# Optimization experiments

Measured on AMD Instinct MI355X. Metric: run time of the kernel, lower is better.

## Reference

```python
import jax, jax.numpy as jnp
import numpy as np
from jax import lax

EPS = 1e-5
HEADS = 4
NPOINT = 512


def _layernorm(x, g, b):
    mu = jnp.mean(x, axis=-1, keepdims=True)
    var = jnp.var(x, axis=-1, keepdims=True)
    return (x - mu) * lax.rsqrt(var + EPS) * g + b


def farthest_point_sample(xyz, npoint):
    # xyz: [B, N, 3] -> idx [B, npoint]  (canonical PointNet++ FPS, seeded at point 0)
    B, N, _ = xyz.shape

    def step(carry, _):
        dist, far = carry  # [B,N], [B]
        centroid = jnp.take_along_axis(xyz, far[:, None, None], axis=1)  # [B,1,3]
        d = jnp.sum((xyz - centroid) ** 2, axis=-1)  # [B,N]
        dist = jnp.minimum(dist, d)
        nxt = jnp.argmax(dist, axis=1).astype(jnp.int32)
        return (dist, nxt), far

    init = (jnp.full((B, N), 1e10, xyz.dtype), jnp.zeros((B,), jnp.int32))
    _, idx = lax.scan(step, init, None, length=npoint)  # [npoint, B]
    return idx.T  # [B, npoint]


def index_points(points, idx):
    # points: [B, N, D], idx: [B, S] -> [B, S, D]
    return jnp.take_along_axis(points, idx[..., None], axis=1)


def setup_inputs() -> dict:
    key = jax.random.key(0)
    ks = iter(jax.random.split(key, 16))
    B, N, Cin, D, Dff, Dout = 8, 2048, 64, 128, 512, 256
    w = lambda k, s: (jax.random.normal(k, s, jnp.float32) * 0.02)
    inp = {
        "xyz": jax.random.normal(next(ks), (B, 3, N), jnp.float32),
        "points": jax.random.normal(next(ks), (B, Cin, N), jnp.float32),
        "W_proj": w(next(ks), (D, Cin)), "b_proj": jnp.zeros((D,)),
        "bn1_g": jnp.ones((D,)), "bn1_b": jnp.zeros((D,)),
        "bn1_m": jnp.zeros((D,)), "bn1_v": jnp.ones((D,)),
        "W_pos": w(next(ks), (D, 3)), "b_pos": jnp.zeros((D,)),
        "Wq": w(next(ks), (D, D)), "bq": jnp.zeros((D,)),
        "Wk": w(next(ks), (D, D)), "bk": jnp.zeros((D,)),
        "Wv": w(next(ks), (D, D)), "bv": jnp.zeros((D,)),
        "Wo": w(next(ks), (D, D)), "bo": jnp.zeros((D,)),
        "ln1_g": jnp.ones((D,)), "ln1_b": jnp.zeros((D,)),
        "W1": w(next(ks), (Dff, D)), "b1": jnp.zeros((Dff,)),
        "W2": w(next(ks), (D, Dff)), "b2": jnp.zeros((D,)),
        "ln2_g": jnp.ones((D,)), "ln2_b": jnp.zeros((D,)),
        "W_fc": w(next(ks), (Dout, D + 3)), "b_fc": jnp.zeros((Dout,)),
        "bn2_g": jnp.ones((Dout,)), "bn2_b": jnp.zeros((Dout,)),
        "bn2_m": jnp.zeros((Dout,)), "bn2_v": jnp.ones((Dout,)),
    }
    return inp


def reference(xyz, points, W_proj, b_proj, bn1_g, bn1_b, bn1_m, bn1_v,
              W_pos, b_pos, Wq, bq, Wk, bk, Wv, bv, Wo, bo,
              ln1_g, ln1_b, W1, b1, W2, b2, ln2_g, ln2_b,
              W_fc, b_fc, bn2_g, bn2_b, bn2_m, bn2_v):
    B, _, N = xyz.shape
    D = W_proj.shape[0]
    hd = D // HEADS

    # project: pointwise conv + BN (inference), output [B, N, D]
    feat = jnp.einsum('dc,bcn->bnd', W_proj, points) + b_proj
    feat = (feat - bn1_m) * lax.rsqrt(bn1_v + EPS) * bn1_g + bn1_b

    # transformer block with xyz positional encoding
    pos = jnp.einsum('dc,bcn->bnd', W_pos, xyz) + b_pos
    x = feat + pos
    q = (x @ Wq.T + bq).reshape(B, N, HEADS, hd)
    k = (x @ Wk.T + bk).reshape(B, N, HEADS, hd)
    v = (x @ Wv.T + bv).reshape(B, N, HEADS, hd)
    scores = jnp.einsum('bnhd,bmhd->bhnm', q, k) / jnp.sqrt(jnp.float32(hd))
    attn = jax.nn.softmax(scores, axis=-1)
    o = jnp.einsum('bhnm,bmhd->bnhd', attn, v).reshape(B, N, D)
    x = _layernorm(x + (o @ Wo.T + bo), ln1_g, ln1_b)
    ffn = jax.nn.relu(x @ W1.T + b1) @ W2.T + b2
    features = _layernorm(x + ffn, ln2_g, ln2_b)  # [B, N, D]

    # sampling + gather
    xyz_t = jnp.transpose(xyz, (0, 2, 1))  # [B, N, 3]
    fps_idx = farthest_point_sample(xyz_t, NPOINT)  # [B, npoint]
    new_points = index_points(features, fps_idx)    # [B, npoint, D]
    new_xyz = index_points(xyz_t, fps_idx)          # [B, npoint, 3]

    cat = jnp.concatenate([new_points, new_xyz], axis=-1)  # [B, npoint, D+3]
    out = jnp.einsum('od,bnd->bon', W_fc, cat) + b_fc[None, :, None]
    out = (out - bn2_m[None, :, None]) * lax.rsqrt(bn2_v + EPS)[None, :, None] \
          * bn2_g[None, :, None] + bn2_b[None, :, None]
    out = jax.nn.relu(out)  # [B, Dout, npoint]

    return jnp.transpose(new_xyz, (0, 2, 1)), out
```

## Files before the change

kernel.cpp:

```cpp
#include <hip/hip_runtime.h>
#include <hip/hip_bf16.h>

#define B_    8
#define N_    2048
#define CIN_  64
#define D_    128
#define DFF_  512
#define DOUT_ 256
#define S_    512
#define H_    4
#define HD_   32
#define EPS_  1e-5f

typedef unsigned short u16;
typedef unsigned long long u64;
typedef __attribute__((ext_vector_type(8))) short short8v;
typedef __attribute__((ext_vector_type(4))) float f32x4;

__device__ __forceinline__ u16 f2bu(float f) {
  __hip_bfloat16 h = __float2bfloat16(f);
  return *(u16*)&h;
}
__device__ __forceinline__ float bu2f(u16 u) {
  __hip_bfloat16 h = *(__hip_bfloat16*)&u;
  return __bfloat162float(h);
}

#define OW_QKV 0
#define OW_O   49152
#define OW_1   65536
#define OW_2   131072
#define OW_FC  196608
#define OW_CAT 237568
#define NW_TOT 249856

__global__ __launch_bounds__(256) void prep_kernel(
    const float* __restrict__ Wq, const float* __restrict__ bq,
    const float* __restrict__ Wk, const float* __restrict__ bk,
    const float* __restrict__ Wv, const float* __restrict__ bv,
    const float* __restrict__ Wo, const float* __restrict__ W1,
    const float* __restrict__ W2, const float* __restrict__ Wfc,
    const float* __restrict__ bfc, const float* __restrict__ Wp,
    const float* __restrict__ bp, const float* __restrict__ Wpos,
    const float* __restrict__ bpos, const float* __restrict__ g1,
    const float* __restrict__ be1, const float* __restrict__ m1,
    const float* __restrict__ v1, const float* __restrict__ g2,
    const float* __restrict__ bb2, const float* __restrict__ m2,
    const float* __restrict__ v2, u16* __restrict__ wb,
    float* __restrict__ fb) {
  const float SC = 0.1767766952966369f;
  int i = blockIdx.x * 256 + threadIdx.x;
  if (i < OW_O) {
    int n = i >> 7, k = i & 127;
    float v = (n < 128) ? Wq[i] * SC
                        : (n < 256) ? Wk[(n - 128) * 128 + k]
                                    : Wv[(n - 256) * 128 + k];
    wb[OW_QKV + i] = f2bu(v);
  } else if (i < OW_1) {
    wb[i] = f2bu(Wo[i - OW_O]);
  } else if (i < OW_2) {
    wb[i] = f2bu(W1[i - OW_1]);
  } else if (i < OW_FC) {
    wb[i] = f2bu(W2[i - OW_2]);
  } else if (i < OW_CAT) {
    int j = i - OW_FC;
    int n = j / 160, c = j % 160;
    wb[i] = f2bu(c < 131 ? Wfc[n * 131 + c] : 0.f);
  } else if (i < NW_TOT) {
    int j = i - OW_CAT;
    int d = j / 96, c = j % 96;
    float v;
    if (c < 64) v = Wp[d * 64 + c] * (g1[d] * rsqrtf(v1[d] + EPS_));
    else if (c < 67) v = Wpos[d * 3 + (c - 64)];
    else v = 0.f;
    wb[i] = f2bu(v);
  } else if (i < NW_TOT + 384) {
    int n = i - NW_TOT;
    fb[n] = (n < 128) ? bq[n] * SC : (n < 256) ? bk[n - 128] : bv[n - 256];
  } else if (i < NW_TOT + 512) {
    int d = i - (NW_TOT + 384);
    float s1 = g1[d] * rsqrtf(v1[d] + EPS_);
    fb[384 + d] = (bp[d] - m1[d]) * s1 + be1[d] + bpos[d];
  } else if (i < NW_TOT + 768) {
    int n = i - (NW_TOT + 512);
    fb[512 + n] = g2[n] * rsqrtf(v2[n] + EPS_);
  } else if (i < NW_TOT + 1024) {
    int n = i - (NW_TOT + 768);
    float s = g2[n] * rsqrtf(v2[n] + EPS_);
    fb[768 + n] = bfc[n] * s + bb2[n] - m2[n] * s;
  }
}

#define FPS_SMEM 256

template <int CTRL, int RM>
__device__ __forceinline__ float dppmax(float v) {
  int m = __builtin_amdgcn_update_dpp(__float_as_int(v), __float_as_int(v),
                                      CTRL, RM, 0xF, true);
  return fmaxf(v, __int_as_float(m));
}

__device__ __forceinline__ void fps_slice(
    char* smem, int b, const float* __restrict__ xyz,
    float* __restrict__ dist_ws, int* __restrict__ far_ws,
    int* __restrict__ idx_out, float* __restrict__ out0, int s0, int s1) {
  u64* keys = (u64*)smem;
  float* crd = (float*)(smem + 64);
  const int t = threadIdx.x, w = t >> 6, lane = t & 63;
  const float* xb = xyz + (size_t)b * 3 * N_;
  const int base = w * 512 + lane * 8;
  float* dw = dist_ws + b * N_;
  float px[8], py[8], pz[8], dist[8];
#pragma unroll
  for (int j = 0; j < 8; j++) {
    px[j] = xb[base + j];
    py[j] = xb[N_ + base + j];
    pz[j] = xb[2 * N_ + base + j];
    dist[j] = 1e10f;
  }
  if (s0 != 0) {
#pragma unroll
    for (int j = 0; j < 8; j++) dist[j] = dw[base + j];
  }
  int far = (s0 == 0) ? 0 : far_ws[b];
  float cx = xb[far], cy = xb[N_ + far], cz = xb[2 * N_ + far];
  for (int s = s0; s < s1; s++) {
    if (t == 0) {
      idx_out[b * S_ + s] = far;
      out0[(size_t)b * 3 * S_ + s] = cx;
      out0[(size_t)b * 3 * S_ + S_ + s] = cy;
      out0[(size_t)b * 3 * S_ + 2 * S_ + s] = cz;
    }
    float best = -1.0f, bx = 0.f, by = 0.f, bz = 0.f;
    int bestp = 0;
#pragma unroll
    for (int j = 0; j < 8; j++) {
      float dx = __fsub_rn(px[j], cx);
      float dy = __fsub_rn(py[j], cy);
      float dz = __fsub_rn(pz[j], cz);
      float d = __fadd_rn(__fadd_rn(__fmul_rn(dx, dx), __fmul_rn(dy, dy)),
                          __fmul_rn(dz, dz));
      float nd = fminf(dist[j], d);
      dist[j] = nd;
      if (nd > best) {
        best = nd; bestp = base + j;
        bx = px[j]; by = py[j]; bz = pz[j];
      }
    }
    float m = best;
    m = dppmax<0x111, 0xF>(m);
    m = dppmax<0x112, 0xF>(m);
    m = dppmax<0x114, 0xF>(m);
    m = dppmax<0x118, 0xF>(m);
    m = dppmax<0x142, 0xA>(m);
    m = dppmax<0x143, 0xC>(m);
    float M = __int_as_float(__builtin_amdgcn_readlane(__float_as_int(m), 63));
    u64 mask = __ballot(best == M);
    int wl = __ffsll((long long)mask) - 1;
    if (lane == wl) {
      int sb = (s & 1) * 4 + w;
      keys[sb] = ((u64)__float_as_uint(M) << 32) |
                 (unsigned)(0xFFFFFFFFu - (unsigned)bestp);
      crd[sb * 3 + 0] = bx;
      crd[sb * 3 + 1] = by;
      crd[sb * 3 + 2] = bz;
    }
    asm volatile("s_waitcnt lgkmcnt(0)" ::: "memory");
    __builtin_amdgcn_s_barrier();
    asm volatile("" ::: "memory");
    const int q0 = (s & 1) * 4;
    u64 k0 = keys[q0], k1 = keys[q0 + 1], k2 = keys[q0 + 2], k3 = keys[q0 + 3];
    float x0 = crd[q0 * 3 + 0], y0 = crd[q0 * 3 + 1], z0 = crd[q0 * 3 + 2];
    float x1 = crd[q0 * 3 + 3], y1 = crd[q0 * 3 + 4], z1 = crd[q0 * 3 + 5];
    float x2 = crd[q0 * 3 + 6], y2 = crd[q0 * 3 + 7], z2 = crd[q0 * 3 + 8];
    float x3 = crd[q0 * 3 + 9], y3 = crd[q0 * 3 + 10], z3 = crd[q0 * 3 + 11];
    bool c01 = k0 >= k1;
    u64 ka = c01 ? k0 : k1;
    float xa = c01 ? x0 : x1, ya = c01 ? y0 : y1, za = c01 ? z0 : z1;
    bool c23 = k2 >= k3;
    u64 kb = c23 ? k2 : k3;
    float xv = c23 ? x2 : x3, yv = c23 ? y2 : y3, zv = c23 ? z2 : z3;
    bool cf = ka >= kb;
    u64 kk = cf ? ka : kb;
    cx = cf ? xa : xv; cy = cf ? ya : yv; cz = cf ? za : zv;
    far = (int)(0xFFFFFFFFu - (unsigned)kk);
  }
#pragma unroll
  for (int j = 0; j < 8; j++) dw[base + j] = dist[j];
  if (t == 0) far_ws[b] = far;
}

template <int K, int KC, int ASTAGE, int EPI>
__global__ __launch_bounds__(256) void gemm_k(
    const u16* __restrict__ A, const u16* __restrict__ W,
    const float* __restrict__ srcf0, const float* __restrict__ srcf1,
    const int* __restrict__ fidx, const float* __restrict__ p0,
    const float* __restrict__ p1, const float* __restrict__ p2,
    const u16* __restrict__ resid, u16* __restrict__ outb,
    float* __restrict__ outf, int ntn, int fpsnb, int s0, int s1,
    const float* fxyz, float* fdist, int* ffar, int* fidxo, float* fout0) {
  constexpr int KP = KC + 8;
  constexpr int GEMM_SMEM = 2 * 128 * KP * 2;
  constexpr int SMEM = GEMM_SMEM > FPS_SMEM ? GEMM_SMEM : FPS_SMEM;
  __shared__ __align__(16) char smem[SMEM];
  if ((int)blockIdx.x < fpsnb) {
    fps_slice(smem, blockIdx.x, fxyz, fdist, ffar, fidxo, fout0, s0, s1);
    return;
  }
  u16 (*As)[KP] = (u16 (*)[KP])smem;
  u16 (*Ws)[KP] = (u16 (*)[KP])(smem + 128 * KP * 2);
  const int bid = blockIdx.x - fpsnb;
  const int mt = bid / ntn, nt = bid % ntn;
  const int t = threadIdx.x, w = t >> 6, lane = t & 63;
  const int g = lane >> 4, lr = lane & 15;

  f32x4 acc[2][8];
#pragma unroll
  for (int qf = 0; qf < 2; qf++)
#pragma unroll
    for (int nf = 0; nf < 8; nf++) acc[qf][nf] = {0.f, 0.f, 0.f, 0.f};

  for (int kc = 0; kc < K / KC; kc++) {
    __syncthreads();
    for (int i = t; i < 128 * (KC / 8); i += 256) {
      int row = i / (KC / 8), c8 = i % (KC / 8);
      *(short8v*)&Ws[row][c8 * 8] =
          *(const short8v*)(W + (size_t)(nt * 128 + row) * K + kc * KC + c8 * 8);
    }
    if constexpr (ASTAGE == 0) {
      for (int i = t; i < 128 * (KC / 8); i += 256) {
        int row = i / (KC / 8), c8 = i % (KC / 8);
        *(short8v*)&As[row][c8 * 8] =
            *(const short8v*)(A + (size_t)(mt * 128 + row) * K + kc * KC + c8 * 8);
      }
    } else if constexpr (ASTAGE == 1) {
      int bb = (mt * 128) >> 11, n0 = (mt * 128) & (N_ - 1);
      for (int i = t; i < 96 * 128; i += 256) {
        int c = i >> 7, n = i & 127;
        float v;
        if (c < 64) v = srcf0[((size_t)bb * CIN_ + c) * N_ + n0 + n];
        else if (c < 67) v = srcf1[((size_t)bb * 3 + (c - 64)) * N_ + n0 + n];
        else v = 0.f;
        As[n][c] = f2bu(v);
      }
    } else {
      int bb = (mt * 128) >> 9, sq0 = (mt * 128) & (S_ - 1);
      for (int i = t; i < 128 * 20; i += 256) {
        int row = i / 20, c8 = i % 20;
        int id = fidx[bb * S_ + sq0 + row];
        short8v val;
        if (c8 < 16) {
          val = *(const short8v*)(A + ((size_t)bb * N_ + id) * D_ + c8 * 8);
        } else if (c8 == 16) {
          val = short8v{0, 0, 0, 0, 0, 0, 0, 0};
          val[0] = (short)f2bu(srcf1[((size_t)bb * 3 + 0) * N_ + id]);
          val[1] = (short)f2bu(srcf1[((size_t)bb * 3 + 1) * N_ + id]);
          val[2] = (short)f2bu(srcf1[((size_t)bb * 3 + 2) * N_ + id]);
        } else {
          val = short8v{0, 0, 0, 0, 0, 0, 0, 0};
        }
        *(short8v*)&As[row][c8 * 8] = val;
      }
    }
    __syncthreads();
#pragma unroll
    for (int ks = 0; ks < KC / 32; ks++) {
      short8v a0 = *(const short8v*)&As[w * 32 + lr][ks * 32 + 8 * g];
      short8v a1 = *(const short8v*)&As[w * 32 + 16 + lr][ks * 32 + 8 * g];
#pragma unroll
      for (int nf = 0; nf < 8; nf++) {
        short8v bb = *(const short8v*)&Ws[nf * 16 + lr][ks * 32 + 8 * g];
        acc[0][nf] = __builtin_amdgcn_mfma_f32_16x16x32_bf16(a0, bb, acc[0][nf], 0, 0, 0);
        acc[1][nf] = __builtin_amdgcn_mfma_f32_16x16x32_bf16(a1, bb, acc[1][nf], 0, 0, 0);
      }
    }
  }

  if constexpr (EPI == 3) {
#pragma unroll
    for (int qf = 0; qf < 2; qf++) {
#pragma unroll
      for (int i = 0; i < 4; i++) {
        int m = mt * 128 + w * 32 + qf * 16 + 4 * g + i;
        float v[8], sm = 0.f, sq = 0.f;
#pragma unroll
        for (int nf = 0; nf < 8; nf++) {
          int n = nf * 16 + lr;
          float x = acc[qf][nf][i] + p0[n] + bu2f(resid[(size_t)m * D_ + n]);
          v[nf] = x;
          sm += x;
          sq += x * x;
        }
#pragma unroll
        for (int msk = 1; msk < 16; msk <<= 1) {
          sm += __shfl_xor(sm, msk);
          sq += __shfl_xor(sq, msk);
        }
        float mu = sm * (1.f / 128.f);
        float var = sq * (1.f / 128.f) - mu * mu;
        float rs = rsqrtf(var + EPS_);
#pragma unroll
        for (int nf = 0; nf < 8; nf++) {
          int n = nf * 16 + lr;
          outb[(size_t)m * D_ + n] = f2bu((v[nf] - mu) * rs * p1[n] + p2[n]);
        }
      }
    }
  } else {
#pragma unroll
    for (int qf = 0; qf < 2; qf++)
#pragma unroll
      for (int nf = 0; nf < 8; nf++)
#pragma unroll
        for (int i = 0; i < 4; i++) {
          int m = mt * 128 + w * 32 + qf * 16 + 4 * g + i;
          int nl = nf * 16 + lr;
          int n = nt * 128 + nl;
          float vv = acc[qf][nf][i];
          if constexpr (EPI == 0) {
            outb[(size_t)m * D_ + nl] = f2bu(vv + p0[n]);
          } else if constexpr (EPI == 1) {
            vv += p0[n];
            int which = n >> 7, h = (n >> 5) & 3, c = n & 31;
            int bb = m >> 11, tok = m & (N_ - 1);
            outb[(size_t)which * 2097152 +
                 (((size_t)bb * H_ + h) * N_ + tok) * HD_ + c] = f2bu(vv);
          } else if constexpr (EPI == 2) {
            outb[(size_t)m * DFF_ + n] = f2bu(fmaxf(vv + p0[n], 0.f));
          } else {
            float r = fmaxf(vv * p1[n] + p2[n], 0.f);
            outf[((size_t)(m >> 9) * DOUT_ + n) * S_ + (m & (S_ - 1))] = r;
          }
        }
  }
}

__global__ __launch_bounds__(256) void attn_mfma_kernel(
    const u16* __restrict__ qg, const u16* __restrict__ kg,
    const u16* __restrict__ vg, u16* __restrict__ o, int fpsnb, int s0, int s1,
    const float* fxyz, float* fdist, int* ffar, int* fidxo, float* fout0) {
  constexpr int ATTN_SMEM = 64 * 40 * 2 + 32 * 72 * 2 + 4 * 16 * 72 * 2;
  constexpr int SMEM = ATTN_SMEM > FPS_SMEM ? ATTN_SMEM : FPS_SMEM;
  __shared__ __align__(16) char smem[SMEM];
  if ((int)blockIdx.x < fpsnb) {
    fps_slice(smem, blockIdx.x, fxyz, fdist, ffar, fidxo, fout0, s0, s1);
    return;
  }
  const int t = threadIdx.x;
  const int w = t >> 6, lane = t & 63, g = lane >> 4, lr = lane & 15;
  u16 (*ks)[40] = (u16 (*)[40])smem;
  u16 (*vt)[72] = (u16 (*)[72])(smem + 5120);
  u16 (*psw)[72] = (u16 (*)[72])(smem + 9728) + w * 16;

  const int bid = blockIdx.x - fpsnb;
  const int qt = bid & 31;
  const int bh = bid >> 5;
  const int b = bh >> 2, h = bh & 3;
  const int qrow = qt * 64 + w * 16 + lr;

  short8v aq = *(const short8v*)(qg + ((size_t)bh * N_ + qrow) * HD_ + 8 * g);

  const u16* kb = kg + (size_t)bh * N_ * HD_;
  const u16* vb = vg + (size_t)bh * N_ * HD_;

  const f32x4 fzero = {0.f, 0.f, 0.f, 0.f};
  float mrun = -INFINITY, lrun = 0.f;
  f32x4 acco[2] = {fzero, fzero};

  const int srow = t >> 2, scol = (t & 3) * 8;

  for (int ch = 0; ch < 32; ch++) {
    __syncthreads();
    short8v kvv = *(const short8v*)(kb + (size_t)(ch * 64 + srow) * HD_ + scol);
    short8v vvv = *(const short8v*)(vb + (size_t)(ch * 64 + srow) * HD_ + scol);
    *(short8v*)(&ks[srow][scol]) = kvv;
#pragma unroll
    for (int e = 0; e < 8; e++) vt[scol + e][srow] = (u16)vvv[e];
    __syncthreads();

    f32x4 st[4];
#pragma unroll
    for (int kt = 0; kt < 4; kt++) {
      short8v ak = *(const short8v*)(&ks[kt * 16 + lr][8 * g]);
      st[kt] = __builtin_amdgcn_mfma_f32_16x16x32_bf16(ak, aq, fzero, 0, 0, 0);
    }

    float mx = -INFINITY;
#pragma unroll
    for (int kt = 0; kt < 4; kt++)
#pragma unroll
      for (int i = 0; i < 4; i++) mx = fmaxf(mx, st[kt][i]);
    mx = fmaxf(mx, __shfl_xor(mx, 16));
    mx = fmaxf(mx, __shfl_xor(mx, 32));
    float nm = fmaxf(mrun, mx);
    float alpha = __expf(mrun - nm);
    mrun = nm;
    float psum = 0.f;
#pragma unroll
    for (int kt = 0; kt < 4; kt++) {
      float p0 = __expf(st[kt][0] - nm);
      float p1 = __expf(st[kt][1] - nm);
      float p2 = __expf(st[kt][2] - nm);
      float p3 = __expf(st[kt][3] - nm);
      psum += (p0 + p1) + (p2 + p3);
      u64 pk = (u64)f2bu(p0) | ((u64)f2bu(p1) << 16) |
               ((u64)f2bu(p2) << 32) | ((u64)f2bu(p3) << 48);
      *(u64*)(&psw[lr][kt * 16 + 4 * g]) = pk;
    }
    psum += __shfl_xor(psum, 16);
    psum += __shfl_xor(psum, 32);
    lrun = lrun * alpha + psum;
#pragma unroll
    for (int dt = 0; dt < 2; dt++)
#pragma unroll
      for (int i = 0; i < 4; i++) acco[dt][i] *= alpha;

#pragma unroll
    for (int mc = 0; mc < 2; mc++) {
      short8v pb = *(const short8v*)(&psw[lr][mc * 32 + 8 * g]);
#pragma unroll
      for (int dt = 0; dt < 2; dt++) {
        short8v av = *(const short8v*)(&vt[dt * 16 + lr][mc * 32 + 8 * g]);
        acco[dt] = __builtin_amdgcn_mfma_f32_16x16x32_bf16(av, pb, acco[dt], 0, 0, 0);
      }
    }
  }

  float rl = 1.0f / lrun;
#pragma unroll
  for (int dt = 0; dt < 2; dt++) {
    u64 pk = (u64)f2bu(acco[dt][0] * rl) | ((u64)f2bu(acco[dt][1] * rl) << 16) |
             ((u64)f2bu(acco[dt][2] * rl) << 32) |
             ((u64)f2bu(acco[dt][3] * rl) << 48);
    *(u64*)(o + ((size_t)b * N_ + qrow) * D_ + h * HD_ + dt * 16 + 4 * g) = pk;
  }
}

extern "C" void kernel_launch(void* const* d_in, const int* in_sizes, int n_in,
                              void* d_out, int out_size, void* d_ws, size_t ws_size,
                              hipStream_t stream) {
  const float* xyz    = (const float*)d_in[0];
  const float* points = (const float*)d_in[1];
  const float* Wp     = (const float*)d_in[2];
  const float* bp     = (const float*)d_in[3];
  const float* g1     = (const float*)d_in[4];
  const float* be1    = (const float*)d_in[5];
  const float* m1     = (const float*)d_in[6];
  const float* v1     = (const float*)d_in[7];
  const float* Wpos   = (const float*)d_in[8];
  const float* bpos   = (const float*)d_in[9];
  const float* Wq     = (const float*)d_in[10];
  const float* bq     = (const float*)d_in[11];
  const float* Wk     = (const float*)d_in[12];
  const float* bk     = (const float*)d_in[13];
  const float* Wv     = (const float*)d_in[14];
  const float* bv     = (const float*)d_in[15];
  const float* Wo     = (const float*)d_in[16];
  const float* bo     = (const float*)d_in[17];
  const float* lg1    = (const float*)d_in[18];
  const float* lb1    = (const float*)d_in[19];
  const float* W1     = (const float*)d_in[20];
  const float* b1     = (const float*)d_in[21];
  const float* W2     = (const float*)d_in[22];
  const float* b2p    = (const float*)d_in[23];
  const float* lg2    = (const float*)d_in[24];
  const float* lb2    = (const float*)d_in[25];
  const float* Wfc    = (const float*)d_in[26];
  const float* bfc    = (const float*)d_in[27];
  const float* g2     = (const float*)d_in[28];
  const float* bb2    = (const float*)d_in[29];
  const float* m2     = (const float*)d_in[30];
  const float* v2     = (const float*)d_in[31];

  float* out0 = (float*)d_out;
  float* out1 = out0 + (size_t)B_ * 3 * S_;

  char* ws = (char*)d_ws;
  int*   fps_idx = (int*)ws;
  u16*   wb      = (u16*)(ws + 16384);
  float* fb      = (float*)(ws + 516096);
  float* dist_ws = (float*)(ws + 520192);
  int*   far_ws  = (int*)(ws + 585728);
  const size_t MB = 1024 * 1024;
  u16* x     = (u16*)(ws + 1 * MB);
  u16* o     = (u16*)(ws + 5 * MB);
  u16* x2    = (u16*)(ws + 9 * MB);
  u16* feats = (u16*)(ws + 13 * MB);
  u16* qb    = (u16*)(ws + 17 * MB);
  u16* h     = (u16*)(ws + 29 * MB);

  prep_kernel<<<980, 256, 0, stream>>>(Wq, bq, Wk, bk, Wv, bv, Wo, W1, W2, Wfc,
                                       bfc, Wp, bp, Wpos, bpos, g1, be1, m1, v1,
                                       g2, bb2, m2, v2, wb, fb);

  gemm_k<96, 96, 1, 0><<<8 + 128, 256, 0, stream>>>(
      nullptr, wb + OW_CAT, points, xyz, nullptr, fb + 384, nullptr, nullptr,
      nullptr, x, nullptr, 1, 8, 0, 70, xyz, dist_ws, far_ws, fps_idx, out0);
  gemm_k<128, 128, 0, 1><<<8 + 384, 256, 0, stream>>>(
      x, wb + OW_QKV, nullptr, nullptr, nullptr, fb, nullptr, nullptr,
      nullptr, qb, nullptr, 3, 8, 70, 160, xyz, dist_ws, far_ws, fps_idx, out0);
  attn_mfma_kernel<<<8 + B_ * H_ * (N_ / 64), 256, 0, stream>>>(
      qb, qb + 2097152, qb + 2 * 2097152, o, 8, 160, 260, xyz, dist_ws, far_ws,
      fps_idx, out0);
  gemm_k<128, 128, 0, 3><<<8 + 128, 256, 0, stream>>>(
      o, wb + OW_O, nullptr, nullptr, nullptr, bo, lg1, lb1, x, x2, nullptr, 1,
      8, 260, 330, xyz, dist_ws, far_ws, fps_idx, out0);
  gemm_k<128, 128, 0, 2><<<8 + 512, 256, 0, stream>>>(
      x2, wb + OW_1, nullptr, nullptr, nullptr, b1, nullptr, nullptr,
      nullptr, h, nullptr, 4, 8, 330, 440, xyz, dist_ws, far_ws, fps_idx, out0);
  gemm_k<512, 128, 0, 3><<<8 + 128, 256, 0, stream>>>(
      h, wb + OW_2, nullptr, nullptr, nullptr, b2p, lg2, lb2, x2, feats,
      nullptr, 1, 8, 440, 512, xyz, dist_ws, far_ws, fps_idx, out0);
  gemm_k<160, 160, 2, 4><<<64, 256, 0, stream>>>(
      feats, wb + OW_FC, nullptr, xyz, fps_idx, nullptr, fb + 512, fb + 768,
      nullptr, nullptr, out1, 2, 0, 0, 0, nullptr, nullptr, nullptr, nullptr,
      nullptr);
}
```

Measured before the change: 360.6 us.

## Rebalance FPS slices, raise FPS wave priority, fold log2e into Q scale

Folds log2(e) into the Q weight and bias scale so the attention softmax uses exp2f instead of __expf. Raises wave priority for the farthest-point-sampling blocks that run alongside the GEMM and attention kernels. Rewrites the cross-wave key reduction as a sequential loop and reassigns how many FPS iterations each co-scheduled kernel carries. The intent is to shorten the FPS critical path that is hidden behind the other kernels and to trim the exponent cost; the changed reduction order and tie comparison could alter tie-breaking semantics.

```diff
diff --git a/kernel.cpp b/kernel.cpp
--- a/kernel.cpp
+++ b/kernel.cpp
@@ -48,7 +48,7 @@
     const float* __restrict__ bb2, const float* __restrict__ m2,
     const float* __restrict__ v2, u16* __restrict__ wb,
     float* __restrict__ fb) {
-  const float SC = 0.1767766952966369f;
+  const float SC = 0.1767766952966369f * 1.4426950408889634f;
   int i = blockIdx.x * 256 + threadIdx.x;
   if (i < OW_O) {
     int n = i >> 7, k = i & 127;
@@ -91,7 +91,7 @@
   }
 }
 
-#define FPS_SMEM 256
+#define FPS_SMEM 320
 
 template <int CTRL, int RM>
 __device__ __forceinline__ float dppmax(float v) {
@@ -106,9 +106,10 @@
     int* __restrict__ idx_out, float* __restrict__ out0, int s0, int s1) {
   u64* keys = (u64*)smem;
   float* crd = (float*)(smem + 64);
+  __builtin_amdgcn_s_setprio(3);
   const int t = threadIdx.x, w = t >> 6, lane = t & 63;
   const float* xb = xyz + (size_t)b * 3 * N_;
-  const int base = w * 512 + lane * 8;
+  const int base = (w * 64 + lane) * 8;
   float* dw = dist_ws + b * N_;
   float px[8], py[8], pz[8], dist[8];
 #pragma unroll
@@ -169,25 +170,24 @@
     __builtin_amdgcn_s_barrier();
     asm volatile("" ::: "memory");
     const int q0 = (s & 1) * 4;
-    u64 k0 = keys[q0], k1 = keys[q0 + 1], k2 = keys[q0 + 2], k3 = keys[q0 + 3];
-    float x0 = crd[q0 * 3 + 0], y0 = crd[q0 * 3 + 1], z0 = crd[q0 * 3 + 2];
-    float x1 = crd[q0 * 3 + 3], y1 = crd[q0 * 3 + 4], z1 = crd[q0 * 3 + 5];
-    float x2 = crd[q0 * 3 + 6], y2 = crd[q0 * 3 + 7], z2 = crd[q0 * 3 + 8];
-    float x3 = crd[q0 * 3 + 9], y3 = crd[q0 * 3 + 10], z3 = crd[q0 * 3 + 11];
-    bool c01 = k0 >= k1;
-    u64 ka = c01 ? k0 : k1;
-    float xa = c01 ? x0 : x1, ya = c01 ? y0 : y1, za = c01 ? z0 : z1;
-    bool c23 = k2 >= k3;
-    u64 kb = c23 ? k2 : k3;
-    float xv = c23 ? x2 : x3, yv = c23 ? y2 : y3, zv = c23 ? z2 : z3;
-    bool cf = ka >= kb;
-    u64 kk = cf ? ka : kb;
-    cx = cf ? xa : xv; cy = cf ? ya : yv; cz = cf ? za : zv;
+    u64 kk = keys[q0];
+    float ccx = crd[q0 * 3], ccy = crd[q0 * 3 + 1], ccz = crd[q0 * 3 + 2];
+#pragma unroll
+    for (int i = 1; i < 4; i++) {
+      u64 ki = keys[q0 + i];
+      bool c = ki > kk;
+      kk = c ? ki : kk;
+      ccx = c ? crd[(q0 + i) * 3] : ccx;
+      ccy = c ? crd[(q0 + i) * 3 + 1] : ccy;
+      ccz = c ? crd[(q0 + i) * 3 + 2] : ccz;
+    }
     far = (int)(0xFFFFFFFFu - (unsigned)kk);
+    cx = ccx; cy = ccy; cz = ccz;
   }
 #pragma unroll
   for (int j = 0; j < 8; j++) dw[base + j] = dist[j];
   if (t == 0) far_ws[b] = far;
+  __builtin_amdgcn_s_setprio(0);
 }
 
 template <int K, int KC, int ASTAGE, int EPI>
@@ -378,30 +378,30 @@
     for (int e = 0; e < 8; e++) vt[scol + e][srow] = (u16)vvv[e];
     __syncthreads();
 
-    f32x4 st[4];
+    f32x4 stv[4];
 #pragma unroll
     for (int kt = 0; kt < 4; kt++) {
       short8v ak = *(const short8v*)(&ks[kt * 16 + lr][8 * g]);
-      st[kt] = __builtin_amdgcn_mfma_f32_16x16x32_bf16(ak, aq, fzero, 0, 0, 0);
+      stv[kt] = __builtin_amdgcn_mfma_f32_16x16x32_bf16(ak, aq, fzero, 0, 0, 0);
     }
 
     float mx = -INFINITY;
 #pragma unroll
     for (int kt = 0; kt < 4; kt++)
 #pragma unroll
-      for (int i = 0; i < 4; i++) mx = fmaxf(mx, st[kt][i]);
+      for (int i = 0; i < 4; i++) mx = fmaxf(mx, stv[kt][i]);
     mx = fmaxf(mx, __shfl_xor(mx, 16));
     mx = fmaxf(mx, __shfl_xor(mx, 32));
     float nm = fmaxf(mrun, mx);
-    float alpha = __expf(mrun - nm);
+    float alpha = exp2f(mrun - nm);
     mrun = nm;
     float psum = 0.f;
 #pragma unroll
     for (int kt = 0; kt < 4; kt++) {
-      float p0 = __expf(st[kt][0] - nm);
-      float p1 = __expf(st[kt][1] - nm);
-      float p2 = __expf(st[kt][2] - nm);
-      float p3 = __expf(st[kt][3] - nm);
+      float p0 = exp2f(stv[kt][0] - nm);
+      float p1 = exp2f(stv[kt][1] - nm);
+      float p2 = exp2f(stv[kt][2] - nm);
+      float p3 = exp2f(stv[kt][3] - nm);
       psum += (p0 + p1) + (p2 + p3);
       u64 pk = (u64)f2bu(p0) | ((u64)f2bu(p1) << 16) |
                ((u64)f2bu(p2) << 32) | ((u64)f2bu(p3) << 48);
@@ -495,22 +495,22 @@
 
   gemm_k<96, 96, 1, 0><<<8 + 128, 256, 0, stream>>>(
       nullptr, wb + OW_CAT, points, xyz, nullptr, fb + 384, nullptr, nullptr,
-      nullptr, x, nullptr, 1, 8, 0, 70, xyz, dist_ws, far_ws, fps_idx, out0);
+      nullptr, x, nullptr, 1, 8, 0, 48, xyz, dist_ws, far_ws, fps_idx, out0);
   gemm_k<128, 128, 0, 1><<<8 + 384, 256, 0, stream>>>(
       x, wb + OW_QKV, nullptr, nullptr, nullptr, fb, nullptr, nullptr,
-      nullptr, qb, nullptr, 3, 8, 70, 160, xyz, dist_ws, far_ws, fps_idx, out0);
+      nullptr, qb, nullptr, 3, 8, 48, 136, xyz, dist_ws, far_ws, fps_idx, out0);
   attn_mfma_kernel<<<8 + B_ * H_ * (N_ / 64), 256, 0, stream>>>(
-      qb, qb + 2097152, qb + 2 * 2097152, o, 8, 160, 260, xyz, dist_ws, far_ws,
+      qb, qb + 2097152, qb + 2 * 2097152, o, 8, 136, 236, xyz, dist_ws, far_ws,
       fps_idx, out0);
   gemm_k<128, 128, 0, 3><<<8 + 128, 256, 0, stream>>>(
       o, wb + OW_O, nullptr, nullptr, nullptr, bo, lg1, lb1, x, x2, nullptr, 1,
-      8, 260, 330, xyz, dist_ws, far_ws, fps_idx, out0);
+      8, 236, 320, xyz, dist_ws, far_ws, fps_idx, out0);
   gemm_k<128, 128, 0, 2><<<8 + 512, 256, 0, stream>>>(
       x2, wb + OW_1, nullptr, nullptr, nullptr, b1, nullptr, nullptr,
-      nullptr, h, nullptr, 4, 8, 330, 440, xyz, dist_ws, far_ws, fps_idx, out0);
+      nullptr, h, nullptr, 4, 8, 320, 420, xyz, dist_ws, far_ws, fps_idx, out0);
   gemm_k<512, 128, 0, 3><<<8 + 128, 256, 0, stream>>>(
       h, wb + OW_2, nullptr, nullptr, nullptr, b2p, lg2, lb2, x2, feats,
-      nullptr, 1, 8, 440, 512, xyz, dist_ws, far_ws, fps_idx, out0);
+      nullptr, 1, 8, 420, 512, xyz, dist_ws, far_ws, fps_idx, out0);
   gemm_k<160, 160, 2, 4><<<64, 256, 0, stream>>>(
       feats, wb + OW_FC, nullptr, xyz, fps_idx, nullptr, fb + 512, fb + 768,
       nullptr, nullptr, out1, 2, 0, 0, 0, nullptr, nullptr, nullptr, nullptr,
```

New measurement: 397.5 us. 1.1x slower.
